# Optimization experiments

Measured on AMD Instinct MI355X. Metric: run time of the kernel, lower is better.

Reference implementation:

```python
import jax, jax.numpy as jnp
import numpy as np

N = 8192
DIMS = 128
HID = 64
NEG = -9e15


def setup_inputs() -> dict:
    key = jax.random.key(0)
    k_adj, k_h, k_w1, k_w2 = jax.random.split(key, 4)
    graph_info = (jax.random.uniform(k_adj, (N, N)) < 0.01).astype(jnp.float32)
    h = jax.random.normal(k_h, (N, DIMS), dtype=jnp.float32)
    # xavier-normal-ish init for the 2-layer scoring MLP (dims -> 64 -> 1)
    W1 = jax.random.normal(k_w1, (DIMS, HID), dtype=jnp.float32) * np.sqrt(2.0 / (DIMS + HID))
    b1 = jnp.zeros((HID,), dtype=jnp.float32)
    W2 = jax.random.normal(k_w2, (HID, 1), dtype=jnp.float32) * np.sqrt(2.0 / (HID + 1))
    b2 = jnp.zeros((1,), dtype=jnp.float32)
    return {"graph_info": graph_info, "h": h, "W1": W1, "b1": b1, "W2": W2, "b2": b2}


def reference(graph_info, h, W1, b1, W2, b2):
    # per-node MLP score: e_j for every node j  -> [N, 1]
    e = jnp.dot(jnp.maximum(jnp.dot(h, W1) + b1, 0.0), W2) + b2
    # e.transpose().repeat(N,1): row i sees scores of all columns j -> broadcast [1, N]
    scores = e[:, 0][None, :]
    # mask non-edges with large negative, softmax over neighbors (dim=-1)
    att = jnp.where(graph_info > 0, scores, jnp.float32(NEG))
    att = jax.nn.softmax(att, axis=-1)
    out = jnp.dot(att, h)  # [N, dims] aggregation
    # sum_flag == 1: rescale each row by its degree (diagflat(num) @ h)
    num = jnp.sum(graph_info, axis=-1)  # [N]
    out = num[:, None] * out
    return out
```

## Files before the change

### kernel.cpp

```cpp
#include <hip/hip_runtime.h>
#include <math.h>

#define NN 8192
#define DIMS 128
#define HID 64
#define CAP 192

typedef float f4v __attribute__((ext_vector_type(4)));
typedef float f2v __attribute__((ext_vector_type(2)));
typedef unsigned long long u64;

__global__ __launch_bounds__(256) void score_kernel(
    const float* __restrict__ h, const float* __restrict__ W1,
    const float* __restrict__ b1, const float* __restrict__ W2,
    const float* __restrict__ b2, float* __restrict__ ee) {
  __shared__ float sW1[DIMS * HID];
  for (int i = threadIdx.x * 4; i < DIMS * HID; i += 1024)
    *(float4*)&sW1[i] = *(const float4*)&W1[i];
  __syncthreads();
  int wv = threadIdx.x >> 6, lane = threadIdx.x & 63;
  int j0 = blockIdx.x * 16 + wv * 4;
  const f4v* h4 = (const f4v*)(h + (size_t)j0 * DIMS);
  float bb = b1[lane];
  float a0 = bb, a1 = bb, a2 = bb, a3 = bb;
#pragma unroll 8
  for (int d4 = 0; d4 < 32; ++d4) {
    f4v v0 = h4[d4], v1 = h4[d4 + 32], v2 = h4[d4 + 64], v3 = h4[d4 + 96];
    float w0 = sW1[(d4 * 4 + 0) * HID + lane];
    float w1 = sW1[(d4 * 4 + 1) * HID + lane];
    float w2c = sW1[(d4 * 4 + 2) * HID + lane];
    float w3 = sW1[(d4 * 4 + 3) * HID + lane];
    a0 = fmaf(v0.x, w0, a0); a0 = fmaf(v0.y, w1, a0); a0 = fmaf(v0.z, w2c, a0); a0 = fmaf(v0.w, w3, a0);
    a1 = fmaf(v1.x, w0, a1); a1 = fmaf(v1.y, w1, a1); a1 = fmaf(v1.z, w2c, a1); a1 = fmaf(v1.w, w3, a1);
    a2 = fmaf(v2.x, w0, a2); a2 = fmaf(v2.y, w1, a2); a2 = fmaf(v2.z, w2c, a2); a2 = fmaf(v2.w, w3, a2);
    a3 = fmaf(v3.x, w0, a3); a3 = fmaf(v3.y, w1, a3); a3 = fmaf(v3.z, w2c, a3); a3 = fmaf(v3.w, w3, a3);
  }
  float w2 = W2[lane];
  float r0 = fmaxf(a0, 0.f) * w2, r1 = fmaxf(a1, 0.f) * w2;
  float r2 = fmaxf(a2, 0.f) * w2, r3 = fmaxf(a3, 0.f) * w2;
#pragma unroll
  for (int off = 32; off > 0; off >>= 1) {
    r0 += __shfl_xor(r0, off, 64);
    r1 += __shfl_xor(r1, off, 64);
    r2 += __shfl_xor(r2, off, 64);
    r3 += __shfl_xor(r3, off, 64);
  }
  if (lane == 0) {
    float bo = b2[0];
    ee[j0]     = expf(r0 + bo);
    ee[j0 + 1] = expf(r1 + bo);
    ee[j0 + 2] = expf(r2 + bo);
    ee[j0 + 3] = expf(r3 + bo);
  }
}


#define NIBBLE(v)                                                              \
  (((__float_as_uint((v).x) >> 29) & 1u) | ((__float_as_uint((v).y) >> 28) & 2u) | \
   ((__float_as_uint((v).z) >> 27) & 4u) | ((__float_as_uint((v).w) >> 26) & 8u))

#define HLD(wj) (*(const float2*)(hbase + ((size_t)__float_as_int((wj).y)) * DIMS))

__global__ __launch_bounds__(256) void agg_kernel(
    const float* __restrict__ graph, const float* __restrict__ h,
    const float* __restrict__ ee, float* __restrict__ out) {
  __shared__ unsigned short s_idx[4][CAP];
  __shared__ float2 s_wj[4][CAP];
  int w = threadIdx.x >> 6;
  int lane = threadIdx.x & 63;
  int row = blockIdx.x * 4 + w;
  const f4v* g4 = (const f4v*)(graph + (size_t)row * NN) + lane;

  u64 acc0 = 0, acc1 = 0;
  f4v p0 = g4[0 * 64], p1 = g4[1 * 64], p2 = g4[2 * 64], p3 = g4[3 * 64];
#pragma unroll
  for (int t = 0; t < 8; ++t) {
    f4v n0, n1, n2, n3;
    if (t < 7) {
      n0 = g4[(t * 4 + 4) * 64];
      n1 = g4[(t * 4 + 5) * 64];
      n2 = g4[(t * 4 + 6) * 64];
      n3 = g4[(t * 4 + 7) * 64];
    }
    {
      u64 q0 = NIBBLE(p0), q1 = NIBBLE(p1), q2 = NIBBLE(p2), q3 = NIBBLE(p3);
      int c = t * 4;
      if (c < 16)      acc0 |= q0 << (4 * (c & 15)); else acc1 |= q0 << (4 * (c & 15));
      if (c + 1 < 16)  acc0 |= q1 << (4 * ((c + 1) & 15)); else acc1 |= q1 << (4 * ((c + 1) & 15));
      if (c + 2 < 16)  acc0 |= q2 << (4 * ((c + 2) & 15)); else acc1 |= q2 << (4 * ((c + 2) & 15));
      if (c + 3 < 16)  acc0 |= q3 << (4 * ((c + 3) & 15)); else acc1 |= q3 << (4 * ((c + 3) & 15));
    }
    if (t < 7) { p0 = n0; p1 = n1; p2 = n2; p3 = n3; }
  }

  int t0 = (int)__popcll(acc0);
  int t1 = (int)__popcll(acc1);
  int tot = t0 + t1;
  int incl = tot;
#pragma unroll
  for (int d = 1; d < 64; d <<= 1) {
    int vsh = __shfl_up(incl, d, 64);
    if (lane >= d) incl += vsh;
  }
  int base = incl - tot;
  int count = __shfl(incl, 63, 64);

  int p = base;
  u64 m = acc0;
  while (m) {
    int b = __ffsll(m) - 1;
    int col = ((b >> 2) << 8) + lane * 4 + (b & 3);
    if (p < CAP) s_idx[w][p] = (unsigned short)col;
    ++p;
    m &= m - 1;
  }
  m = acc1;
  while (m) {
    int b = __ffsll(m) - 1;
    int col = 4096 + ((b >> 2) << 8) + lane * 4 + (b & 3);
    if (p < CAP) s_idx[w][p] = (unsigned short)col;
    ++p;
    m &= m - 1;
  }
  if (count > CAP) count = CAP;

  float z = 0.f;
  for (int q = lane; q < count; q += 64) {
    int j = s_idx[w][q];
    float wv = ee[j];
    s_wj[w][q] = make_float2(wv, __int_as_float(j));
    z += wv;
  }
#pragma unroll
  for (int off = 32; off > 0; off >>= 1) z += __shfl_xor(z, off, 64);

  float ax = 0.f, ay = 0.f;
  const float* hbase = h + lane * 2;
  int q = 0;
  int n8 = count & ~7;
  for (; q < n8; q += 8) {
    float2 wj0 = s_wj[w][q + 0], wj1 = s_wj[w][q + 1];
    float2 wj2 = s_wj[w][q + 2], wj3 = s_wj[w][q + 3];
    float2 wj4 = s_wj[w][q + 4], wj5 = s_wj[w][q + 5];
    float2 wj6 = s_wj[w][q + 6], wj7 = s_wj[w][q + 7];
    float2 h0 = HLD(wj0), h1 = HLD(wj1), h2 = HLD(wj2), h3 = HLD(wj3);
    float2 h4 = HLD(wj4), h5 = HLD(wj5), h6 = HLD(wj6), h7 = HLD(wj7);
    ax = fmaf(wj0.x, h0.x, ax); ay = fmaf(wj0.x, h0.y, ay);
    ax = fmaf(wj1.x, h1.x, ax); ay = fmaf(wj1.x, h1.y, ay);
    ax = fmaf(wj2.x, h2.x, ax); ay = fmaf(wj2.x, h2.y, ay);
    ax = fmaf(wj3.x, h3.x, ax); ay = fmaf(wj3.x, h3.y, ay);
    ax = fmaf(wj4.x, h4.x, ax); ay = fmaf(wj4.x, h4.y, ay);
    ax = fmaf(wj5.x, h5.x, ax); ay = fmaf(wj5.x, h5.y, ay);
    ax = fmaf(wj6.x, h6.x, ax); ay = fmaf(wj6.x, h6.y, ay);
    ax = fmaf(wj7.x, h7.x, ax); ay = fmaf(wj7.x, h7.y, ay);
  }
  for (; q < count; ++q) {
    float2 wj = s_wj[w][q];
    float2 hv = HLD(wj);
    ax = fmaf(wj.x, hv.x, ax);
    ay = fmaf(wj.x, hv.y, ay);
  }
  float scale = (count > 0) ? ((float)count / z) : 0.f;
  f2v o2;
  o2.x = ax * scale;
  o2.y = ay * scale;
  __builtin_nontemporal_store(o2, (f2v*)(out + (size_t)row * DIMS + lane * 2));
}

extern "C" void kernel_launch(void* const* d_in, const int* in_sizes, int n_in,
                              void* d_out, int out_size, void* d_ws, size_t ws_size,
                              hipStream_t stream) {
  const float* graph = (const float*)d_in[0];
  const float* h     = (const float*)d_in[1];
  const float* W1    = (const float*)d_in[2];
  const float* b1    = (const float*)d_in[3];
  const float* W2    = (const float*)d_in[4];
  const float* b2    = (const float*)d_in[5];
  float* out = (float*)d_out;
  float* ee  = (float*)d_ws;

  score_kernel<<<NN / 16, 256, 0, stream>>>(h, W1, b1, W2, b2, ee);
  agg_kernel<<<NN / 4, 256, 0, stream>>>(graph, h, ee, out);
}
```

Before: 76.54 us.

## Replace sparse gather aggregation with dense fp16 MFMA GEMM over adjacency

Drops the per-row bitmask compaction and sparse gather of h rows. Adds a pre-pass that builds a transposed fp16 matrix of exp-weighted h rows, with extra columns for count and softmax normaliser. Then runs a dense MFMA GEMM of the full adjacency (converted to fp16 in registers) against it, with split-K across waves and a shared-memory reduction. The main read, the 256MB adjacency, is the same, but it now does dense tensor-core math and fp16 rounding of the weighted features. That rounding can cost accuracy.

```diff
diff --git a/kernel.cpp b/kernel.cpp
--- a/kernel.cpp
+++ b/kernel.cpp
@@ -4,11 +4,11 @@
 #define NN 8192
 #define DIMS 128
 #define HID 64
-#define CAP 192
+#define NF 9
 
 typedef float f4v __attribute__((ext_vector_type(4)));
-typedef float f2v __attribute__((ext_vector_type(2)));
-typedef unsigned long long u64;
+typedef float f32x4 __attribute__((ext_vector_type(4)));
+typedef _Float16 f16x8 __attribute__((ext_vector_type(8)));
 
 __global__ __launch_bounds__(256) void score_kernel(
     const float* __restrict__ h, const float* __restrict__ W1,
@@ -54,117 +54,136 @@
   }
 }
 
-
-#define NIBBLE(v)                                                              \
-  (((__float_as_uint((v).x) >> 29) & 1u) | ((__float_as_uint((v).y) >> 28) & 2u) | \
-   ((__float_as_uint((v).z) >> 27) & 4u) | ((__float_as_uint((v).w) >> 26) & 8u))
-
-#define HLD(wj) (*(const float2*)(hbase + ((size_t)__float_as_int((wj).y)) * DIMS))
-
-__global__ __launch_bounds__(256) void agg_kernel(
-    const float* __restrict__ graph, const float* __restrict__ h,
-    const float* __restrict__ ee, float* __restrict__ out) {
-  __shared__ unsigned short s_idx[4][CAP];
-  __shared__ float2 s_wj[4][CAP];
-  int w = threadIdx.x >> 6;
-  int lane = threadIdx.x & 63;
-  int row = blockIdx.x * 4 + w;
-  const f4v* g4 = (const f4v*)(graph + (size_t)row * NN) + lane;
-
-  u64 acc0 = 0, acc1 = 0;
-  f4v p0 = g4[0 * 64], p1 = g4[1 * 64], p2 = g4[2 * 64], p3 = g4[3 * 64];
-#pragma unroll
-  for (int t = 0; t < 8; ++t) {
-    f4v n0, n1, n2, n3;
-    if (t < 7) {
-      n0 = g4[(t * 4 + 4) * 64];
-      n1 = g4[(t * 4 + 5) * 64];
-      n2 = g4[(t * 4 + 6) * 64];
-      n3 = g4[(t * 4 + 7) * 64];
+__global__ __launch_bounds__(256) void bt_kernel(
+    const float* __restrict__ h, const float* __restrict__ ee,
+    _Float16* __restrict__ Bt) {
+  __shared__ float sh[64][129];
+  __shared__ float see[64];
+  int jb = blockIdx.x * 64;
+  for (int i = threadIdx.x; i < 64 * 32; i += 256) {
+    int r = i >> 5, c4 = i & 31;
+    float4 v = *(const float4*)(h + (size_t)(jb + r) * DIMS + c4 * 4);
+    sh[r][c4 * 4 + 0] = v.x; sh[r][c4 * 4 + 1] = v.y;
+    sh[r][c4 * 4 + 2] = v.z; sh[r][c4 * 4 + 3] = v.w;
+  }
+  if (threadIdx.x < 64) see[threadIdx.x] = ee[jb + threadIdx.x];
+  __syncthreads();
+  int g = threadIdx.x >> 6, j = threadIdx.x & 63;
+  float eej = see[j];
+  for (int d = g; d < 16 * NF; d += 4) {
+    float v;
+    if (d < 128) v = sh[j][d] * eej;
+    else if (d == 128) v = 1.0f;
+    else if (d == 129) v = eej;
+    else v = 0.0f;
+    Bt[(size_t)d * NN + jb + j] = (_Float16)v;
+  }
+}
+
+__device__ __forceinline__ f16x8 cvt8(f32x4 lo, f32x4 hi) {
+  f16x8 r;
+  r[0] = (_Float16)lo[0]; r[1] = (_Float16)lo[1];
+  r[2] = (_Float16)lo[2]; r[3] = (_Float16)lo[3];
+  r[4] = (_Float16)hi[0]; r[5] = (_Float16)hi[1];
+  r[6] = (_Float16)hi[2]; r[7] = (_Float16)hi[3];
+  return r;
+}
+
+__global__ __launch_bounds__(256) void gemm_kernel(
+    const float* __restrict__ graph, const _Float16* __restrict__ Bt,
+    float* __restrict__ out) {
+  __shared__ float red[3][32][145];
+  __shared__ float cz[2][32];
+  int w = threadIdx.x >> 6, l = threadIdx.x & 63;
+  int lw = l & 15, lh = l >> 4;
+  int rb = blockIdx.x * 32;
+
+  const float* A0p = graph + (size_t)(rb + lw) * NN + lh * 8;
+  const float* A1p = A0p + (size_t)16 * NN;
+  const _Float16* Bp = Bt + (size_t)lw * NN + lh * 8;
+
+  f32x4 acc[2][NF];
+#pragma unroll
+  for (int m = 0; m < 2; ++m)
+#pragma unroll
+    for (int n = 0; n < NF; ++n) acc[m][n] = (f32x4)(0.f);
+
+  int k = w * 2048;
+  f32x4 ca0, ca1, ca2, ca3, na0, na1, na2, na3;
+  f16x8 cb[NF], nb[NF];
+  ca0 = *(const f32x4*)(A0p + k); ca1 = *(const f32x4*)(A0p + k + 4);
+  ca2 = *(const f32x4*)(A1p + k); ca3 = *(const f32x4*)(A1p + k + 4);
+#pragma unroll
+  for (int n = 0; n < NF; ++n) cb[n] = *(const f16x8*)(Bp + (size_t)n * 16 * NN + k);
+
+#pragma unroll 2
+  for (int s = 0; s < 64; ++s) {
+    if (s < 63) {
+      na0 = *(const f32x4*)(A0p + k + 32); na1 = *(const f32x4*)(A0p + k + 36);
+      na2 = *(const f32x4*)(A1p + k + 32); na3 = *(const f32x4*)(A1p + k + 36);
+#pragma unroll
+      for (int n = 0; n < NF; ++n)
+        nb[n] = *(const f16x8*)(Bp + (size_t)n * 16 * NN + k + 32);
     }
-    {
-      u64 q0 = NIBBLE(p0), q1 = NIBBLE(p1), q2 = NIBBLE(p2), q3 = NIBBLE(p3);
-      int c = t * 4;
-      if (c < 16)      acc0 |= q0 << (4 * (c & 15)); else acc1 |= q0 << (4 * (c & 15));
-      if (c + 1 < 16)  acc0 |= q1 << (4 * ((c + 1) & 15)); else acc1 |= q1 << (4 * ((c + 1) & 15));
-      if (c + 2 < 16)  acc0 |= q2 << (4 * ((c + 2) & 15)); else acc1 |= q2 << (4 * ((c + 2) & 15));
-      if (c + 3 < 16)  acc0 |= q3 << (4 * ((c + 3) & 15)); else acc1 |= q3 << (4 * ((c + 3) & 15));
+    f16x8 af0 = cvt8(ca0, ca1);
+    f16x8 af1 = cvt8(ca2, ca3);
+#pragma unroll
+    for (int n = 0; n < NF; ++n) {
+      acc[0][n] = __builtin_amdgcn_mfma_f32_16x16x32_f16(af0, cb[n], acc[0][n], 0, 0, 0);
+      acc[1][n] = __builtin_amdgcn_mfma_f32_16x16x32_f16(af1, cb[n], acc[1][n], 0, 0, 0);
     }
-    if (t < 7) { p0 = n0; p1 = n1; p2 = n2; p3 = n3; }
-  }
-
-  int t0 = (int)__popcll(acc0);
-  int t1 = (int)__popcll(acc1);
-  int tot = t0 + t1;
-  int incl = tot;
-#pragma unroll
-  for (int d = 1; d < 64; d <<= 1) {
-    int vsh = __shfl_up(incl, d, 64);
-    if (lane >= d) incl += vsh;
-  }
-  int base = incl - tot;
-  int count = __shfl(incl, 63, 64);
-
-  int p = base;
-  u64 m = acc0;
-  while (m) {
-    int b = __ffsll(m) - 1;
-    int col = ((b >> 2) << 8) + lane * 4 + (b & 3);
-    if (p < CAP) s_idx[w][p] = (unsigned short)col;
-    ++p;
-    m &= m - 1;
-  }
-  m = acc1;
-  while (m) {
-    int b = __ffsll(m) - 1;
-    int col = 4096 + ((b >> 2) << 8) + lane * 4 + (b & 3);
-    if (p < CAP) s_idx[w][p] = (unsigned short)col;
-    ++p;
-    m &= m - 1;
-  }
-  if (count > CAP) count = CAP;
-
-  float z = 0.f;
-  for (int q = lane; q < count; q += 64) {
-    int j = s_idx[w][q];
-    float wv = ee[j];
-    s_wj[w][q] = make_float2(wv, __int_as_float(j));
-    z += wv;
-  }
-#pragma unroll
-  for (int off = 32; off > 0; off >>= 1) z += __shfl_xor(z, off, 64);
-
-  float ax = 0.f, ay = 0.f;
-  const float* hbase = h + lane * 2;
-  int q = 0;
-  int n8 = count & ~7;
-  for (; q < n8; q += 8) {
-    float2 wj0 = s_wj[w][q + 0], wj1 = s_wj[w][q + 1];
-    float2 wj2 = s_wj[w][q + 2], wj3 = s_wj[w][q + 3];
-    float2 wj4 = s_wj[w][q + 4], wj5 = s_wj[w][q + 5];
-    float2 wj6 = s_wj[w][q + 6], wj7 = s_wj[w][q + 7];
-    float2 h0 = HLD(wj0), h1 = HLD(wj1), h2 = HLD(wj2), h3 = HLD(wj3);
-    float2 h4 = HLD(wj4), h5 = HLD(wj5), h6 = HLD(wj6), h7 = HLD(wj7);
-    ax = fmaf(wj0.x, h0.x, ax); ay = fmaf(wj0.x, h0.y, ay);
-    ax = fmaf(wj1.x, h1.x, ax); ay = fmaf(wj1.x, h1.y, ay);
-    ax = fmaf(wj2.x, h2.x, ax); ay = fmaf(wj2.x, h2.y, ay);
-    ax = fmaf(wj3.x, h3.x, ax); ay = fmaf(wj3.x, h3.y, ay);
-    ax = fmaf(wj4.x, h4.x, ax); ay = fmaf(wj4.x, h4.y, ay);
-    ax = fmaf(wj5.x, h5.x, ax); ay = fmaf(wj5.x, h5.y, ay);
-    ax = fmaf(wj6.x, h6.x, ax); ay = fmaf(wj6.x, h6.y, ay);
-    ax = fmaf(wj7.x, h7.x, ax); ay = fmaf(wj7.x, h7.y, ay);
-  }
-  for (; q < count; ++q) {
-    float2 wj = s_wj[w][q];
-    float2 hv = HLD(wj);
-    ax = fmaf(wj.x, hv.x, ax);
-    ay = fmaf(wj.x, hv.y, ay);
-  }
-  float scale = (count > 0) ? ((float)count / z) : 0.f;
-  f2v o2;
-  o2.x = ax * scale;
-  o2.y = ay * scale;
-  __builtin_nontemporal_store(o2, (f2v*)(out + (size_t)row * DIMS + lane * 2));
+    ca0 = na0; ca1 = na1; ca2 = na2; ca3 = na3;
+#pragma unroll
+    for (int n = 0; n < NF; ++n) cb[n] = nb[n];
+    k += 32;
+  }
+
+  if (w > 0) {
+#pragma unroll
+    for (int m = 0; m < 2; ++m)
+#pragma unroll
+      for (int n = 0; n < NF; ++n)
+#pragma unroll
+        for (int r = 0; r < 4; ++r)
+          red[w - 1][m * 16 + lh * 4 + r][n * 16 + lw] = acc[m][n][r];
+  }
+  __syncthreads();
+  if (w == 0) {
+#pragma unroll
+    for (int m = 0; m < 2; ++m)
+#pragma unroll
+      for (int n = 0; n < NF; ++n)
+#pragma unroll
+        for (int r = 0; r < 4; ++r) {
+          int rr = m * 16 + lh * 4 + r, cc = n * 16 + lw;
+          acc[m][n][r] += red[0][rr][cc] + red[1][rr][cc] + red[2][rr][cc];
+        }
+    if (lw < 2) {
+#pragma unroll
+      for (int m = 0; m < 2; ++m)
+#pragma unroll
+        for (int r = 0; r < 4; ++r)
+          cz[lw][m * 16 + lh * 4 + r] = acc[m][NF - 1][r];
+    }
+    asm volatile("s_waitcnt lgkmcnt(0)" ::: "memory");
+    float sc[2][4];
+#pragma unroll
+    for (int m = 0; m < 2; ++m)
+#pragma unroll
+      for (int r = 0; r < 4; ++r) {
+        float cnt = cz[0][m * 16 + lh * 4 + r];
+        float zz  = cz[1][m * 16 + lh * 4 + r];
+        sc[m][r] = cnt > 0.f ? cnt / zz : 0.f;
+      }
+#pragma unroll
+    for (int m = 0; m < 2; ++m)
+#pragma unroll
+      for (int n = 0; n < 8; ++n)
+#pragma unroll
+        for (int r = 0; r < 4; ++r)
+          out[(size_t)(rb + m * 16 + lh * 4 + r) * DIMS + n * 16 + lw] =
+              acc[m][n][r] * sc[m][r];
+  }
 }
 
 extern "C" void kernel_launch(void* const* d_in, const int* in_sizes, int n_in,
@@ -177,8 +196,11 @@
   const float* W2    = (const float*)d_in[4];
   const float* b2    = (const float*)d_in[5];
   float* out = (float*)d_out;
-  float* ee  = (float*)d_ws;
+
+  float* ee = (float*)d_ws;
+  _Float16* Bt = (_Float16*)((char*)d_ws + NN * sizeof(float));
 
   score_kernel<<<NN / 16, 256, 0, stream>>>(h, W1, b1, W2, b2, ee);
-  agg_kernel<<<NN / 4, 256, 0, stream>>>(graph, h, ee, out);
-}
+  bt_kernel<<<NN / 64, 256, 0, stream>>>(h, ee, Bt);
+  gemm_kernel<<<NN / 32, 256, 0, stream>>>(graph, Bt, out);
+}
```

After: 134.7 us. 76.0% more time.

## Software-pipeline adjacency scan with neighbor gather across rows per wave

Applied to the files above, without the earlier changes.

The aggregation kernel becomes persistent-style: each wave handles four rows, and while it streams the next row's adjacency it gathers h rows for the previous row's neighbors. Index lists sit in double-buffered LDS. The separate LDS weight-staging pass is dropped, and the softmax denominator is accumulated inside the gather. This aims to overlap the dominant 256MB graph read with the latency-bound gather, at the cost of four times fewer blocks, and it swaps the nontemporal output store for a plain one.

```diff
diff --git a/kernel.cpp b/kernel.cpp
--- a/kernel.cpp
+++ b/kernel.cpp
@@ -5,9 +5,13 @@
 #define DIMS 128
 #define HID 64
 #define CAP 192
+#define NWAVES 4
+#define NPHASE 4
+#define WTOT 2048
 
 typedef float f4v __attribute__((ext_vector_type(4)));
 typedef float f2v __attribute__((ext_vector_type(2)));
+typedef unsigned short u16x8 __attribute__((ext_vector_type(8)));
 typedef unsigned long long u64;
 
 __global__ __launch_bounds__(256) void score_kernel(
@@ -56,115 +60,120 @@
 
 
 #define NIBBLE(v)                                                              \
-  (((__float_as_uint((v).x) >> 29) & 1u) | ((__float_as_uint((v).y) >> 28) & 2u) | \
-   ((__float_as_uint((v).z) >> 27) & 4u) | ((__float_as_uint((v).w) >> 26) & 8u))
+  ((u64)(((__float_as_uint((v).x) >> 29) & 1u) |                               \
+         ((__float_as_uint((v).y) >> 28) & 2u) |                               \
+         ((__float_as_uint((v).z) >> 27) & 4u) |                               \
+         ((__float_as_uint((v).w) >> 26) & 8u)))
 
-#define HLD(wj) (*(const float2*)(hbase + ((size_t)__float_as_int((wj).y)) * DIMS))
+__device__ __forceinline__ void gather_batch8(
+    const unsigned short* sidx, int q, int cnt,
+    const float* __restrict__ ee, const float* __restrict__ hb,
+    float& ax, float& ay, float& z) {
+  if (q >= cnt) return;
+  u16x8 jv = *(const u16x8*)(sidx + q);
+  int j[8];
+#pragma unroll
+  for (int k = 0; k < 8; ++k) j[k] = (q + k < cnt) ? (int)jv[k] : 0;
+  float wv[8];
+#pragma unroll
+  for (int k = 0; k < 8; ++k) wv[k] = ee[j[k]];
+  f2v hv[8];
+#pragma unroll
+  for (int k = 0; k < 8; ++k) hv[k] = *(const f2v*)(hb + (size_t)j[k] * DIMS);
+#pragma unroll
+  for (int k = 0; k < 8; ++k) {
+    float m = (q + k < cnt) ? wv[k] : 0.f;
+    z += m;
+    ax = fmaf(m, hv[k].x, ax);
+    ay = fmaf(m, hv[k].y, ay);
+  }
+}
 
-__global__ __launch_bounds__(256) void agg_kernel(
+__global__ __launch_bounds__(256) void fused_kernel(
     const float* __restrict__ graph, const float* __restrict__ h,
     const float* __restrict__ ee, float* __restrict__ out) {
-  __shared__ unsigned short s_idx[4][CAP];
-  __shared__ float2 s_wj[4][CAP];
-  int w = threadIdx.x >> 6;
-  int lane = threadIdx.x & 63;
-  int row = blockIdx.x * 4 + w;
-  const f4v* g4 = (const f4v*)(graph + (size_t)row * NN) + lane;
+  __shared__ unsigned short s_idx[NWAVES][2][CAP];
+  int w = threadIdx.x >> 6, lane = threadIdx.x & 63;
+  int g = blockIdx.x * NWAVES + w;
+  const float* hb = h + lane * 2;
+  u64 lt = (1ull << lane) - 1ull;
 
-  u64 acc0 = 0, acc1 = 0;
-  f4v p0 = g4[0 * 64], p1 = g4[1 * 64], p2 = g4[2 * 64], p3 = g4[3 * 64];
+  int pcnt = 0, pbuf = 0, prow = 0;
+  float ax = 0.f, ay = 0.f, z = 0.f;
+
+#pragma unroll 1
+  for (int p = 0; p < NPHASE; ++p) {
+    int row = g + p * WTOT;
+    const f4v* g4 = (const f4v*)(graph + (size_t)row * NN) + lane;
+    u64 a0 = 0, a1 = 0;
+    f4v c0 = g4[0], c1 = g4[64], c2 = g4[128], c3 = g4[192];
 #pragma unroll
-  for (int t = 0; t < 8; ++t) {
-    f4v n0, n1, n2, n3;
-    if (t < 7) {
-      n0 = g4[(t * 4 + 4) * 64];
-      n1 = g4[(t * 4 + 5) * 64];
-      n2 = g4[(t * 4 + 6) * 64];
-      n3 = g4[(t * 4 + 7) * 64];
+    for (int t = 0; t < 8; ++t) {
+      f4v n0, n1, n2, n3;
+      if (t < 7) {
+        const f4v* nb2 = g4 + (t * 4 + 4) * 64;
+        n0 = nb2[0]; n1 = nb2[64]; n2 = nb2[128]; n3 = nb2[192];
+      }
+      {
+        u64 q0 = NIBBLE(c0), q1 = NIBBLE(c1), q2 = NIBBLE(c2), q3 = NIBBLE(c3);
+        int c = t * 4;
+        if (c < 16)     a0 |= q0 << (4 * (c & 15));       else a1 |= q0 << (4 * (c & 15));
+        if (c + 1 < 16) a0 |= q1 << (4 * ((c + 1) & 15)); else a1 |= q1 << (4 * ((c + 1) & 15));
+        if (c + 2 < 16) a0 |= q2 << (4 * ((c + 2) & 15)); else a1 |= q2 << (4 * ((c + 2) & 15));
+        if (c + 3 < 16) a0 |= q3 << (4 * ((c + 3) & 15)); else a1 |= q3 << (4 * ((c + 3) & 15));
+      }
+      if (p > 0) {
+        gather_batch8(&s_idx[w][pbuf][0], t * 16 + 0, pcnt, ee, hb, ax, ay, z);
+        gather_batch8(&s_idx[w][pbuf][0], t * 16 + 8, pcnt, ee, hb, ax, ay, z);
+      }
+      if (t < 7) { c0 = n0; c1 = n1; c2 = n2; c3 = n3; }
+    }
+    if (p > 0) {
+#pragma unroll 1
+      for (int q = 128; q < pcnt; q += 8)
+        gather_batch8(&s_idx[w][pbuf][0], q, pcnt, ee, hb, ax, ay, z);
+      float scale = pcnt > 0 ? (float)pcnt / z : 0.f;
+      f2v o2; o2.x = ax * scale; o2.y = ay * scale;
+      *(f2v*)(out + (size_t)prow * DIMS + lane * 2) = o2;
     }
     {
-      u64 q0 = NIBBLE(p0), q1 = NIBBLE(p1), q2 = NIBBLE(p2), q3 = NIBBLE(p3);
-      int c = t * 4;
-      if (c < 16)      acc0 |= q0 << (4 * (c & 15)); else acc1 |= q0 << (4 * (c & 15));
-      if (c + 1 < 16)  acc0 |= q1 << (4 * ((c + 1) & 15)); else acc1 |= q1 << (4 * ((c + 1) & 15));
-      if (c + 2 < 16)  acc0 |= q2 << (4 * ((c + 2) & 15)); else acc1 |= q2 << (4 * ((c + 2) & 15));
-      if (c + 3 < 16)  acc0 |= q3 << (4 * ((c + 3) & 15)); else acc1 |= q3 << (4 * ((c + 3) & 15));
+      int t0 = (int)__popcll(a0), t1 = (int)__popcll(a1);
+      int tot = t0 + t1, incl = tot;
+#pragma unroll
+      for (int d = 1; d < 64; d <<= 1) {
+        int vsh = __shfl_up(incl, d, 64);
+        if (lane >= d) incl += vsh;
+      }
+      int base = incl - tot;
+      int cnt = __shfl(incl, 63, 64);
+      unsigned short* dst = &s_idx[w][p & 1][0];
+      int pidx = base;
+      u64 m = a0;
+      while (m) {
+        int bit = __ffsll(m) - 1;
+        int col = ((bit >> 2) << 8) + lane * 4 + (bit & 3);
+        if (pidx < CAP) dst[pidx] = (unsigned short)col;
+        ++pidx; m &= m - 1;
+      }
+      m = a1;
+      while (m) {
+        int bit = __ffsll(m) - 1;
+        int col = 4096 + ((bit >> 2) << 8) + lane * 4 + (bit & 3);
+        if (pidx < CAP) dst[pidx] = (unsigned short)col;
+        ++pidx; m &= m - 1;
+      }
+      pcnt = cnt < CAP ? cnt : CAP;
+      pbuf = p & 1;
+      prow = row;
+      ax = 0.f; ay = 0.f; z = 0.f;
     }
-    if (t < 7) { p0 = n0; p1 = n1; p2 = n2; p3 = n3; }
   }
-
-  int t0 = (int)__popcll(acc0);
-  int t1 = (int)__popcll(acc1);
-  int tot = t0 + t1;
-  int incl = tot;
-#pragma unroll
-  for (int d = 1; d < 64; d <<= 1) {
-    int vsh = __shfl_up(incl, d, 64);
-    if (lane >= d) incl += vsh;
-  }
-  int base = incl - tot;
-  int count = __shfl(incl, 63, 64);
-
-  int p = base;
-  u64 m = acc0;
-  while (m) {
-    int b = __ffsll(m) - 1;
-    int col = ((b >> 2) << 8) + lane * 4 + (b & 3);
-    if (p < CAP) s_idx[w][p] = (unsigned short)col;
-    ++p;
-    m &= m - 1;
-  }
-  m = acc1;
-  while (m) {
-    int b = __ffsll(m) - 1;
-    int col = 4096 + ((b >> 2) << 8) + lane * 4 + (b & 3);
-    if (p < CAP) s_idx[w][p] = (unsigned short)col;
-    ++p;
-    m &= m - 1;
-  }
-  if (count > CAP) count = CAP;
-
-  float z = 0.f;
-  for (int q = lane; q < count; q += 64) {
-    int j = s_idx[w][q];
-    float wv = ee[j];
-    s_wj[w][q] = make_float2(wv, __int_as_float(j));
-    z += wv;
-  }
-#pragma unroll
-  for (int off = 32; off > 0; off >>= 1) z += __shfl_xor(z, off, 64);
-
-  float ax = 0.f, ay = 0.f;
-  const float* hbase = h + lane * 2;
-  int q = 0;
-  int n8 = count & ~7;
-  for (; q < n8; q += 8) {
-    float2 wj0 = s_wj[w][q + 0], wj1 = s_wj[w][q + 1];
-    float2 wj2 = s_wj[w][q + 2], wj3 = s_wj[w][q + 3];
-    float2 wj4 = s_wj[w][q + 4], wj5 = s_wj[w][q + 5];
-    float2 wj6 = s_wj[w][q + 6], wj7 = s_wj[w][q + 7];
-    float2 h0 = HLD(wj0), h1 = HLD(wj1), h2 = HLD(wj2), h3 = HLD(wj3);
-    float2 h4 = HLD(wj4), h5 = HLD(wj5), h6 = HLD(wj6), h7 = HLD(wj7);
-    ax = fmaf(wj0.x, h0.x, ax); ay = fmaf(wj0.x, h0.y, ay);
-    ax = fmaf(wj1.x, h1.x, ax); ay = fmaf(wj1.x, h1.y, ay);
-    ax = fmaf(wj2.x, h2.x, ax); ay = fmaf(wj2.x, h2.y, ay);
-    ax = fmaf(wj3.x, h3.x, ax); ay = fmaf(wj3.x, h3.y, ay);
-    ax = fmaf(wj4.x, h4.x, ax); ay = fmaf(wj4.x, h4.y, ay);
-    ax = fmaf(wj5.x, h5.x, ax); ay = fmaf(wj5.x, h5.y, ay);
-    ax = fmaf(wj6.x, h6.x, ax); ay = fmaf(wj6.x, h6.y, ay);
-    ax = fmaf(wj7.x, h7.x, ax); ay = fmaf(wj7.x, h7.y, ay);
-  }
-  for (; q < count; ++q) {
-    float2 wj = s_wj[w][q];
-    float2 hv = HLD(wj);
-    ax = fmaf(wj.x, hv.x, ax);
-    ay = fmaf(wj.x, hv.y, ay);
-  }
-  float scale = (count > 0) ? ((float)count / z) : 0.f;
-  f2v o2;
-  o2.x = ax * scale;
-  o2.y = ay * scale;
-  __builtin_nontemporal_store(o2, (f2v*)(out + (size_t)row * DIMS + lane * 2));
+#pragma unroll 1
+  for (int q = 0; q < pcnt; q += 8)
+    gather_batch8(&s_idx[w][pbuf][0], q, pcnt, ee, hb, ax, ay, z);
+  float scale = pcnt > 0 ? (float)pcnt / z : 0.f;
+  f2v o2; o2.x = ax * scale; o2.y = ay * scale;
+  *(f2v*)(out + (size_t)prow * DIMS + lane * 2) = o2;
 }
 
 extern "C" void kernel_launch(void* const* d_in, const int* in_sizes, int n_in,
@@ -180,5 +189,5 @@
   float* ee  = (float*)d_ws;
 
   score_kernel<<<NN / 16, 256, 0, stream>>>(h, W1, b1, W2, b2, ee);
-  agg_kernel<<<NN / 4, 256, 0, stream>>>(graph, h, ee, out);
+  fused_kernel<<<WTOT / NWAVES, 256, 0, stream>>>(graph, h, ee, out);
 }
```

New measurement: 78.98 us. 3.2% more time.
